# Kernel optimization log

Measured on AMD Instinct MI355X. Metric: run time of the kernel, lower is better.

Reference implementation:

```python
import jax, jax.numpy as jnp
import numpy as np

N_FILTERS = 1024
N_HEADS = 8  # hardcoded h=8 in the original einops.rearrange
LN_EPS = 1e-3  # keras LayerNormalization default epsilon


def setup_inputs() -> dict:
    key = jax.random.key(0)
    k1, k2, k3 = jax.random.split(key, 3)
    B, N, C = 4, 2048, N_FILTERS
    x = jax.random.normal(k1, (B, N, C), dtype=jnp.float32)
    ln_gamma = jnp.ones((C,), dtype=jnp.float32)
    ln_beta = jnp.zeros((C,), dtype=jnp.float32)
    w_qkv = jax.random.normal(k2, (C, 3 * C), dtype=jnp.float32) * 0.02
    w_out = jax.random.normal(k3, (C, C), dtype=jnp.float32) * 0.02
    b_out = jnp.zeros((C,), dtype=jnp.float32)
    return {"x": x, "ln_gamma": ln_gamma, "ln_beta": ln_beta,
            "w_qkv": w_qkv, "w_out": w_out, "b_out": b_out}


def reference(x, ln_gamma, ln_beta, w_qkv, w_out, b_out):
    B, N, C = x.shape
    h = N_HEADS
    hd = C // h
    scale = jnp.asarray(float(C) ** (-0.5), dtype=x.dtype)  # note: full C, as in source

    # LayerNorm over last axis (keras default)
    mu = jnp.mean(x, axis=-1, keepdims=True)
    var = jnp.var(x, axis=-1, keepdims=True)
    xn = (x - mu) / jnp.sqrt(var + LN_EPS) * ln_gamma + ln_beta

    # QKV projection (no bias): [B, N, 3C]
    qkv = jnp.einsum('bnc,cd->bnd', xn, w_qkv)
    # rearrange 'b n (qkv h c) -> qkv b h n c'
    qkv = qkv.reshape(B, N, 3, h, hd).transpose(2, 0, 3, 1, 4)
    q, k, v = qkv[0], qkv[1], qkv[2]

    # attention: [B, h, N, N]
    scores = jnp.einsum('bhnc,bhmc->bhnm', q, k) * scale
    attn = jax.nn.softmax(scores, axis=-1)
    out = jnp.einsum('bhnm,bhmc->bhnc', attn, v)
    # 'b h n c -> b n (h c)'
    out = out.transpose(0, 2, 1, 3).reshape(B, N, C)

    out = jnp.einsum('bnc,cd->bnd', out, w_out) + b_out
    return x + out
```

## Files before the change

kernel.cpp:

```cpp
#include <hip/hip_runtime.h>

typedef _Float16 half8 __attribute__((ext_vector_type(8)));
typedef float floatx4 __attribute__((ext_vector_type(4)));
typedef float floatx16 __attribute__((ext_vector_type(16)));

#define BB 4
#define SEQ 2048
#define CHN 1024
#define NH 8
#define HD 128
#define CQ 3072

__device__ __forceinline__ float bf2f(unsigned short b) {
  unsigned int u = ((unsigned int)b) << 16;
  float f; __builtin_memcpy(&f, &u, 4); return f;
}
__device__ __forceinline__ unsigned short f2bf(float f) {
  unsigned int u; __builtin_memcpy(&u, &f, 4);
  u += 0x7fffu + ((u >> 16) & 1u);
  return (unsigned short)(u >> 16);
}
__device__ __forceinline__ void gl_lds16(const _Float16* g, _Float16* l) {
  __builtin_amdgcn_global_load_lds(
      (const __attribute__((address_space(1))) unsigned int*)(g),
      (__attribute__((address_space(3))) unsigned int*)(l), 16, 0, 0);
}
__device__ __forceinline__ unsigned int pkf16(float a, float b) {
  auto p = __builtin_amdgcn_cvt_pkrtz(a, b);
  unsigned int u; __builtin_memcpy(&u, &p, 4); return u;
}

__global__ __launch_bounds__(256) void detect_k(
    const unsigned int* __restrict__ x, int* __restrict__ flag) {
  __shared__ int bad;
  if (threadIdx.x == 0) bad = 0;
  __syncthreads();
  int b = 0;
#pragma unroll
  for (int i = 0; i < 8; ++i) {
    unsigned int w = x[threadIdx.x * 8 + i];
    float v = bf2f((unsigned short)(w & 0xffffu));
    if (!(fabsf(v) < 1e4f)) b = 1;
  }
  if (b) bad = 1;
  __syncthreads();
  if (threadIdx.x == 0) *flag = bad;
}

__global__ __launch_bounds__(256) void transpose_b2h(
    const void* __restrict__ in, _Float16* __restrict__ out, int R, int C,
    const int* __restrict__ flag) {
  __shared__ _Float16 tile[64][66];
  int isf = *flag;
  int ti = blockIdx.y, tj = blockIdx.x, t = threadIdx.x;
  if (isf) {
    const float* inf = (const float*)in;
#pragma unroll
    for (int i = 0; i < 16; ++i) {
      int lin = i * 256 + t;
      int r = lin >> 6, c = lin & 63;
      tile[r][c] = (_Float16)inf[(size_t)(ti * 64 + r) * C + tj * 64 + c];
    }
  } else {
    const unsigned short* inb = (const unsigned short*)in;
#pragma unroll
    for (int i = 0; i < 16; ++i) {
      int lin = i * 256 + t;
      int r = lin >> 6, c = lin & 63;
      tile[r][c] = (_Float16)bf2f(inb[(size_t)(ti * 64 + r) * C + tj * 64 + c]);
    }
  }
  __syncthreads();
#pragma unroll
  for (int i = 0; i < 16; ++i) {
    int lin = i * 256 + t;
    int c = lin >> 6, r = lin & 63;
    out[(size_t)(tj * 64 + c) * R + ti * 64 + r] = tile[r][c];
  }
}

__global__ __launch_bounds__(256) void ln_k(
    const void* __restrict__ xv, const void* __restrict__ gv,
    const void* __restrict__ bv, _Float16* __restrict__ xn,
    const int* __restrict__ flag) {
  int isf = *flag;
  int row = blockIdx.x, t = threadIdx.x;
  float v0, v1, v2, v3;
  if (isf) {
    const float4 f = *reinterpret_cast<const float4*>((const float*)xv + (size_t)row * CHN + t * 4);
    v0 = f.x; v1 = f.y; v2 = f.z; v3 = f.w;
  } else {
    ushort4 u = *reinterpret_cast<const ushort4*>((const unsigned short*)xv + (size_t)row * CHN + t * 4);
    v0 = bf2f(u.x); v1 = bf2f(u.y); v2 = bf2f(u.z); v3 = bf2f(u.w);
  }
  float s = v0 + v1 + v2 + v3;
  float ss = v0 * v0 + v1 * v1 + v2 * v2 + v3 * v3;
#pragma unroll
  for (int off = 32; off >= 1; off >>= 1) {
    s += __shfl_xor(s, off, 64);
    ss += __shfl_xor(ss, off, 64);
  }
  __shared__ float red[8];
  int wave = t >> 6, lane = t & 63;
  if (lane == 0) { red[wave] = s; red[4 + wave] = ss; }
  __syncthreads();
  s = red[0] + red[1] + red[2] + red[3];
  ss = red[4] + red[5] + red[6] + red[7];
  float mu = s * (1.0f / CHN);
  float var = ss * (1.0f / CHN) - mu * mu;
  float rstd = rsqrtf(var + 1e-3f);
  float g0, g1, g2, g3, b0, b1, b2, b3;
  if (isf) {
    const float4 g = *reinterpret_cast<const float4*>((const float*)gv + t * 4);
    const float4 b = *reinterpret_cast<const float4*>((const float*)bv + t * 4);
    g0 = g.x; g1 = g.y; g2 = g.z; g3 = g.w;
    b0 = b.x; b1 = b.y; b2 = b.z; b3 = b.w;
  } else {
    ushort4 g = *reinterpret_cast<const ushort4*>((const unsigned short*)gv + t * 4);
    ushort4 b = *reinterpret_cast<const ushort4*>((const unsigned short*)bv + t * 4);
    g0 = bf2f(g.x); g1 = bf2f(g.y); g2 = bf2f(g.z); g3 = bf2f(g.w);
    b0 = bf2f(b.x); b1 = bf2f(b.y); b2 = bf2f(b.z); b3 = bf2f(b.w);
  }
  _Float16* o = xn + (size_t)row * CHN + t * 4;
  o[0] = (_Float16)((v0 - mu) * rstd * g0 + b0);
  o[1] = (_Float16)((v1 - mu) * rstd * g1 + b1);
  o[2] = (_Float16)((v2 - mu) * rstd * g2 + b2);
  o[3] = (_Float16)((v3 - mu) * rstd * g3 + b3);
}

template <int EPI>
__global__ __launch_bounds__(256, 3) void gemm_k(
    const _Float16* __restrict__ A, const _Float16* __restrict__ Bt,
    int M, int Nn, int K,
    _Float16* __restrict__ outh, void* __restrict__ outv,
    const void* __restrict__ bias, const void* __restrict__ resid,
    const int* __restrict__ flag) {
  __shared__ _Float16 As[128 * 64];
  __shared__ _Float16 Bs[128 * 64];
  int isf = (EPI == 1) ? *flag : 0;
  int t = threadIdx.x;
  int wave = t >> 6, lane = t & 63, quad = lane >> 4, l15 = lane & 15;
  int wm = wave >> 1, wn = wave & 1;
  size_t arow0 = (size_t)blockIdx.y * 128;
  size_t brow0 = (size_t)blockIdx.x * 128;
  int lr = lane >> 3, lc = lane & 7;
  int gc = lc ^ lr;
  const _Float16* Abase = A + (arow0 + wave * 32 + lr) * (size_t)K + gc * 8;
  const _Float16* Bbase = Bt + (brow0 + wave * 32 + lr) * (size_t)K + gc * 8;
  floatx4 acc[4][4] = {};
  int nkt = K >> 6;
  for (int kt = 0; kt < nkt; ++kt) {
#pragma unroll
    for (int i = 0; i < 4; ++i) {
      gl_lds16(Abase + kt * 64 + (size_t)i * 8 * K, As + (wave * 32 + i * 8) * 64);
      gl_lds16(Bbase + kt * 64 + (size_t)i * 8 * K, Bs + (wave * 32 + i * 8) * 64);
    }
    __syncthreads();
#pragma unroll
    for (int ks = 0; ks < 2; ++ks) {
      half8 af[4], bfr[4];
#pragma unroll
      for (int mt = 0; mt < 4; ++mt) {
        int row = wm * 64 + mt * 16 + l15;
        int slot = (ks * 4 + quad) ^ (l15 & 7);
        af[mt] = *reinterpret_cast<const half8*>(As + row * 64 + slot * 8);
      }
#pragma unroll
      for (int nt = 0; nt < 4; ++nt) {
        int row = wn * 64 + nt * 16 + l15;
        int slot = (ks * 4 + quad) ^ (l15 & 7);
        bfr[nt] = *reinterpret_cast<const half8*>(Bs + row * 64 + slot * 8);
      }
#pragma unroll
      for (int mt = 0; mt < 4; ++mt)
#pragma unroll
        for (int nt = 0; nt < 4; ++nt)
          acc[mt][nt] = __builtin_amdgcn_mfma_f32_16x16x32_f16(af[mt], bfr[nt], acc[mt][nt], 0, 0, 0);
    }
    __syncthreads();
  }
#pragma unroll
  for (int mt = 0; mt < 4; ++mt) {
#pragma unroll
    for (int r = 0; r < 4; ++r) {
      size_t row = arow0 + wm * 64 + mt * 16 + quad * 4 + r;
#pragma unroll
      for (int nt = 0; nt < 4; ++nt) {
        size_t col = brow0 + wn * 64 + nt * 16 + l15;
        float v = acc[mt][nt][r];
        if (EPI == 0) {
          outh[row * Nn + col] = (_Float16)v;
        } else {
          if (isf) {
            v += ((const float*)bias)[col] + ((const float*)resid)[row * Nn + col];
            ((float*)outv)[row * Nn + col] = v;
          } else {
            v += bf2f(((const unsigned short*)bias)[col]) +
                 bf2f(((const unsigned short*)resid)[row * Nn + col]);
            ((unsigned short*)outv)[row * Nn + col] = f2bf(v);
          }
        }
      }
    }
  }
}

__global__ __launch_bounds__(256) void vtrans_k(
    const _Float16* __restrict__ qkv, _Float16* __restrict__ vtr) {
  __shared__ _Float16 tile[64][72];
  int t = threadIdx.x;
  int tok0 = blockIdx.x * 64;
  int hd0 = blockIdx.y * 64;
  int bh = blockIdx.z;
  int b = bh >> 3, h = bh & 7;
  const _Float16* src = qkv + (size_t)b * SEQ * CQ + 2 * CHN + h * HD + hd0;
#pragma unroll
  for (int i = 0; i < 2; ++i) {
    int lin = i * 256 + t;
    int r = lin >> 3, c8 = lin & 7;
    *reinterpret_cast<half8*>(&tile[r][c8 * 8]) =
        *reinterpret_cast<const half8*>(src + (size_t)(tok0 + r) * CQ + c8 * 8);
  }
  __syncthreads();
  _Float16* dst = vtr + ((size_t)bh * HD + hd0) * SEQ + tok0;
#pragma unroll
  for (int i = 0; i < 2; ++i) {
    int lin = i * 256 + t;
    int c = lin >> 3, r8 = lin & 7;
    half8 v;
#pragma unroll
    for (int j = 0; j < 8; ++j) v[j] = tile[r8 * 8 + j][c];
    *reinterpret_cast<half8*>(dst + (size_t)c * SEQ + r8 * 8) = v;
  }
}

__global__ __launch_bounds__(256, 2) void attn_k(
    const _Float16* __restrict__ qkv, const _Float16* __restrict__ vtr,
    _Float16* __restrict__ out) {
  __shared__ _Float16 Ks[2][64 * 128];
  __shared__ _Float16 Vs[2][128 * 64];
  int t = threadIdx.x;
  int wave = t >> 6, lane = t & 63;
  int l31 = lane & 31, hi = lane >> 5;
  int bh = blockIdx.x & 31;
  int qt = blockIdx.x >> 5;
  int b = bh >> 3, h = bh & 7;
  int qbase = qt * 128;
  const _Float16* qp = qkv + (size_t)b * SEQ * CQ + h * HD;
  const _Float16* kp = qp + CHN;
  const _Float16* vtp = vtr + (size_t)bh * HD * SEQ;
  const _Float16 qsc = (_Float16)0.045085299f;
  half8 aq[8];
  {
    const _Float16* qr = qp + (size_t)(qbase + wave * 32 + l31) * CQ + hi * 8;
#pragma unroll
    for (int c = 0; c < 8; ++c) {
      half8 v = *reinterpret_cast<const half8*>(qr + c * 16);
#pragma unroll
      for (int j = 0; j < 8; ++j) v[j] = v[j] * qsc;
      aq[c] = v;
    }
  }
  float l_p = 0.0f;
  floatx16 accO[4] = {};
  int kr = lane >> 4, ks16 = lane & 15;
  int vr = lane >> 3, vs8 = lane & 7;
#pragma unroll
  for (int i = 0; i < 4; ++i) {
    int r = wave * 16 + i * 4 + kr;
    int gcs = ks16 ^ (r & 15);
    gl_lds16(kp + (size_t)r * CQ + gcs * 8, Ks[0] + (wave * 16 + i * 4) * 128);
  }
#pragma unroll
  for (int i = 0; i < 4; ++i) {
    int r = wave * 32 + i * 8 + vr;
    int gcs = vs8 ^ (r & 7);
    gl_lds16(vtp + (size_t)r * SEQ + gcs * 8, Vs[0] + (wave * 32 + i * 8) * 64);
  }
  __syncthreads();
  for (int kt = 0; kt < SEQ / 64; ++kt) {
    if (kt + 1 < SEQ / 64) {
      int kb2 = (kt + 1) * 64;
      _Float16* vdst = Vs[(kt + 1) & 1];
#pragma unroll
      for (int i = 0; i < 4; ++i) {
        int r = wave * 32 + i * 8 + vr;
        int gcs = vs8 ^ (r & 7);
        gl_lds16(vtp + (size_t)r * SEQ + kb2 + gcs * 8, vdst + (wave * 32 + i * 8) * 64);
      }
      const _Float16* kn = kp + (size_t)kb2 * CQ;
      _Float16* kdst = Ks[(kt + 1) & 1];
#pragma unroll
      for (int i = 0; i < 4; ++i) {
        int r = wave * 16 + i * 4 + kr;
        int gcs = ks16 ^ (r & 15);
        gl_lds16(kn + (size_t)r * CQ + gcs * 8, kdst + (wave * 16 + i * 4) * 128);
      }
    }
    const _Float16* kc = Ks[kt & 1];
    floatx16 accST[2] = {};
    __builtin_amdgcn_s_setprio(1);
#pragma unroll
    for (int c = 0; c < 8; ++c) {
#pragma unroll
      for (int sub = 0; sub < 2; ++sub) {
        int row = sub * 32 + l31;
        int chunk = (c * 2 + hi) ^ (row & 15);
        half8 ak = *reinterpret_cast<const half8*>(kc + row * 128 + chunk * 8);
        accST[sub] = __builtin_amdgcn_mfma_f32_32x32x16_f16(ak, aq[c], accST[sub], 0, 0, 0);
      }
    }
    __builtin_amdgcn_s_setprio(0);
    float p0[16], p1[16];
#pragma unroll
    for (int r = 0; r < 16; ++r) p0[r] = __builtin_amdgcn_exp2f(accST[0][r]);
#pragma unroll
    for (int r = 0; r < 16; ++r) p1[r] = __builtin_amdgcn_exp2f(accST[1][r]);
    {
      float s0 = 0, s1 = 0, s2 = 0, s3 = 0;
#pragma unroll
      for (int r = 0; r < 16; r += 4) {
        s0 += p0[r] + p1[r];
        s1 += p0[r + 1] + p1[r + 1];
        s2 += p0[r + 2] + p1[r + 2];
        s3 += p0[r + 3] + p1[r + 3];
      }
      l_p += (s0 + s1) + (s2 + s3);
    }
    const _Float16* vc = Vs[kt & 1];
    __builtin_amdgcn_s_setprio(1);
#pragma unroll
    for (int s = 0; s < 4; ++s) {
      const float* pp = (s & 2) ? p1 : p0;
      int o8 = (s & 1) * 8;
      unsigned int u0 = pkf16(pp[o8 + 0], pp[o8 + 1]);
      unsigned int u1 = pkf16(pp[o8 + 2], pp[o8 + 3]);
      unsigned int w0 = pkf16(pp[o8 + 4], pp[o8 + 5]);
      unsigned int w1 = pkf16(pp[o8 + 6], pp[o8 + 7]);
      asm volatile("v_permlane32_swap_b32 %0, %1" : "+v"(u0), "+v"(w0));
      asm volatile("v_permlane32_swap_b32 %0, %1" : "+v"(u1), "+v"(w1));
      union { unsigned int w[4]; half8 h; } fr;
      fr.w[0] = u0; fr.w[1] = u1; fr.w[2] = w0; fr.w[3] = w1;
#pragma unroll
      for (int dt = 0; dt < 4; ++dt) {
        int row = dt * 32 + l31;
        int chunk = (2 * s + hi) ^ (row & 7);
        half8 bv = *reinterpret_cast<const half8*>(vc + row * 64 + chunk * 8);
        accO[dt] = __builtin_amdgcn_mfma_f32_32x32x16_f16(fr.h, bv, accO[dt], 0, 0, 0);
      }
    }
    __builtin_amdgcn_s_setprio(0);
    __syncthreads();
  }
  l_p += __shfl_xor(l_p, 32, 64);
  float inv[16];
#pragma unroll
  for (int r = 0; r < 16; ++r) {
    int qrow = (r & 3) + 8 * (r >> 2) + 4 * hi;
    inv[r] = 1.0f / __shfl(l_p, qrow, 64);
  }
  _Float16* obase = out + ((size_t)b * SEQ + qbase + wave * 32) * CHN + h * HD;
#pragma unroll
  for (int dt = 0; dt < 4; ++dt)
#pragma unroll
    for (int r = 0; r < 16; ++r) {
      int qrow = (r & 3) + 8 * (r >> 2) + 4 * hi;
      obase[(size_t)qrow * CHN + dt * 32 + l31] = (_Float16)(accO[dt][r] * inv[r]);
    }
}

extern "C" void kernel_launch(void* const* d_in, const int* in_sizes, int n_in,
                              void* d_out, int out_size, void* d_ws, size_t ws_size,
                              hipStream_t stream) {
  (void)in_sizes; (void)n_in; (void)out_size; (void)ws_size;
  const void* x = d_in[0];
  const void* gam = d_in[1];
  const void* bet = d_in[2];
  const void* wqkv = d_in[3];
  const void* wout = d_in[4];
  const void* bout = d_in[5];
  char* ws = (char*)d_ws;
  _Float16* xn    = (_Float16*)(ws);
  _Float16* vtr   = (_Float16*)(ws);
  _Float16* qkv   = (_Float16*)(ws + (size_t)16777216);
  _Float16* aout  = (_Float16*)(ws + (size_t)67108864);
  _Float16* wqkvT = (_Float16*)(ws + (size_t)83886080);
  _Float16* woutT = (_Float16*)(ws + (size_t)90177536);
  int* flag       = (int*)(ws + (size_t)92274688);

  detect_k<<<1, 256, 0, stream>>>((const unsigned int*)x, flag);
  transpose_b2h<<<dim3(CQ / 64, CHN / 64), 256, 0, stream>>>(wqkv, wqkvT, CHN, CQ, flag);
  transpose_b2h<<<dim3(CHN / 64, CHN / 64), 256, 0, stream>>>(wout, woutT, CHN, CHN, flag);
  ln_k<<<dim3(BB * SEQ), 256, 0, stream>>>(x, gam, bet, xn, flag);
  gemm_k<0><<<dim3(CQ / 128, BB * SEQ / 128), 256, 0, stream>>>(
      xn, wqkvT, BB * SEQ, CQ, CHN, qkv, nullptr, nullptr, nullptr, flag);
  vtrans_k<<<dim3(SEQ / 64, HD / 64, BB * NH), 256, 0, stream>>>(qkv, vtr);
  attn_k<<<dim3(BB * NH * (SEQ / 128)), 256, 0, stream>>>(qkv, vtr, aout);
  gemm_k<1><<<dim3(CHN / 128, BB * SEQ / 128), 256, 0, stream>>>(
      aout, woutT, BB * SEQ, CHN, CHN, nullptr, d_out, bout, x, flag);
}
```

Before: 295.0 us.

## Triple-buffer GEMM with 256x128 tiles, 512 threads and swizzled block order

Reworks the projection GEMM into a 256x128 output tile computed by 8 waves, using a K-step of 32. Global-to-LDS loads now go through a three-stage ring buffer whose waits are counted with explicit vmcnt, so loads run two steps ahead of the MFMA work. Blocks are remapped in groups of eight to improve L2 reuse. The attention kernel's LDS index expressions are only rewritten into an equivalent form. The changes add hand-tuned wait counts and larger LDS use, and the swizzle assumes the grid size divides evenly by eight.

```diff
diff --git a/kernel.cpp b/kernel.cpp
--- a/kernel.cpp
+++ b/kernel.cpp
@@ -129,55 +129,77 @@
 }
 
 template <int EPI>
-__global__ __launch_bounds__(256, 3) void gemm_k(
+__global__ __launch_bounds__(512, 2) void gemm_k(
     const _Float16* __restrict__ A, const _Float16* __restrict__ Bt,
     int M, int Nn, int K,
     _Float16* __restrict__ outh, void* __restrict__ outv,
     const void* __restrict__ bias, const void* __restrict__ resid,
     const int* __restrict__ flag) {
-  __shared__ _Float16 As[128 * 64];
-  __shared__ _Float16 Bs[128 * 64];
+  __shared__ _Float16 As[3][256 * 32];
+  __shared__ _Float16 Bs[3][128 * 32];
   int isf = (EPI == 1) ? *flag : 0;
   int t = threadIdx.x;
   int wave = t >> 6, lane = t & 63, quad = lane >> 4, l15 = lane & 15;
   int wm = wave >> 1, wn = wave & 1;
-  size_t arow0 = (size_t)blockIdx.y * 128;
-  size_t brow0 = (size_t)blockIdx.x * 128;
-  int lr = lane >> 3, lc = lane & 7;
-  int gc = lc ^ lr;
-  const _Float16* Abase = A + (arow0 + wave * 32 + lr) * (size_t)K + gc * 8;
-  const _Float16* Bbase = Bt + (brow0 + wave * 32 + lr) * (size_t)K + gc * 8;
+  int nbx = Nn >> 7;
+  int bid = blockIdx.x;
+  int swz = (bid & 7) * ((int)gridDim.x >> 3) + (bid >> 3);
+  int by = swz / nbx;
+  int bx = swz - by * nbx;
+  size_t arow0 = (size_t)by * 256;
+  size_t brow0 = (size_t)bx * 128;
+  int lr = lane >> 2, lc = lane & 3;
+  int gsw = lc ^ ((lr >> 1) & 3);
+  int slotr = quad ^ ((l15 >> 1) & 3);
+
+  auto stage = [&](int kt, int bufi) {
+    int k0 = kt << 5;
+#pragma unroll
+    for (int j = 0; j < 2; ++j) {
+      int r0 = wave * 32 + j * 16;
+      gl_lds16(A + (arow0 + r0 + lr) * (size_t)K + k0 + gsw * 8,
+               &As[bufi][r0 * 32]);
+    }
+    {
+      int r0 = wave * 16;
+      gl_lds16(Bt + (brow0 + r0 + lr) * (size_t)K + k0 + gsw * 8,
+               &Bs[bufi][r0 * 32]);
+    }
+  };
+
   floatx4 acc[4][4] = {};
-  int nkt = K >> 6;
+  int nkt = K >> 5;
+  stage(0, 0);
+  stage(1, 1);
+  stage(2, 2);
+  int bufc = 0;
   for (int kt = 0; kt < nkt; ++kt) {
-#pragma unroll
-    for (int i = 0; i < 4; ++i) {
-      gl_lds16(Abase + kt * 64 + (size_t)i * 8 * K, As + (wave * 32 + i * 8) * 64);
-      gl_lds16(Bbase + kt * 64 + (size_t)i * 8 * K, Bs + (wave * 32 + i * 8) * 64);
-    }
-    __syncthreads();
-#pragma unroll
-    for (int ks = 0; ks < 2; ++ks) {
-      half8 af[4], bfr[4];
-#pragma unroll
-      for (int mt = 0; mt < 4; ++mt) {
-        int row = wm * 64 + mt * 16 + l15;
-        int slot = (ks * 4 + quad) ^ (l15 & 7);
-        af[mt] = *reinterpret_cast<const half8*>(As + row * 64 + slot * 8);
-      }
-#pragma unroll
-      for (int nt = 0; nt < 4; ++nt) {
-        int row = wn * 64 + nt * 16 + l15;
-        int slot = (ks * 4 + quad) ^ (l15 & 7);
-        bfr[nt] = *reinterpret_cast<const half8*>(Bs + row * 64 + slot * 8);
-      }
-#pragma unroll
-      for (int mt = 0; mt < 4; ++mt)
-#pragma unroll
-        for (int nt = 0; nt < 4; ++nt)
-          acc[mt][nt] = __builtin_amdgcn_mfma_f32_16x16x32_f16(af[mt], bfr[nt], acc[mt][nt], 0, 0, 0);
-    }
-    __syncthreads();
+    if (kt < nkt - 2)       asm volatile("s_waitcnt vmcnt(6)" ::: "memory");
+    else if (kt == nkt - 2) asm volatile("s_waitcnt vmcnt(3)" ::: "memory");
+    else                    asm volatile("s_waitcnt vmcnt(0)" ::: "memory");
+    asm volatile("s_waitcnt lgkmcnt(0)" ::: "memory");
+    __builtin_amdgcn_sched_barrier(0);
+    __builtin_amdgcn_s_barrier();
+    __builtin_amdgcn_sched_barrier(0);
+    if (kt + 2 < nkt) {
+      int bn = bufc + 2; if (bn >= 3) bn -= 3;
+      stage(kt + 2, bn);
+    }
+    const _Float16* Ab = As[bufc];
+    const _Float16* Bb = Bs[bufc];
+    half8 af[4], bf[4];
+#pragma unroll
+    for (int mt = 0; mt < 4; ++mt)
+      af[mt] = *reinterpret_cast<const half8*>(Ab + (wm * 64 + mt * 16 + l15) * 32 + slotr * 8);
+#pragma unroll
+    for (int nt = 0; nt < 4; ++nt)
+      bf[nt] = *reinterpret_cast<const half8*>(Bb + (wn * 64 + nt * 16 + l15) * 32 + slotr * 8);
+#pragma unroll
+    for (int mt = 0; mt < 4; ++mt)
+#pragma unroll
+      for (int nt = 0; nt < 4; ++nt)
+        acc[mt][nt] = __builtin_amdgcn_mfma_f32_16x16x32_f16(af[mt], bf[nt], acc[mt][nt], 0, 0, 0);
+    ++bufc; if (bufc == 3) bufc = 0;
   }
 #pragma unroll
   for (int mt = 0; mt < 4; ++mt) {
@@ -306,7 +328,7 @@
       for (int sub = 0; sub < 2; ++sub) {
         int row = sub * 32 + l31;
         int chunk = (c * 2 + hi) ^ (row & 15);
-        half8 ak = *reinterpret_cast<const half8*>(kc + row * 128 + chunk * 8);
+        half8 ak = *reinterpret_cast<const half8*>(kc + (row * 16 + chunk) * 8);
         accST[sub] = __builtin_amdgcn_mfma_f32_32x32x16_f16(ak, aq[c], accST[sub], 0, 0, 0);
       }
     }
@@ -345,7 +367,7 @@
       for (int dt = 0; dt < 4; ++dt) {
         int row = dt * 32 + l31;
         int chunk = (2 * s + hi) ^ (row & 7);
-        half8 bv = *reinterpret_cast<const half8*>(vc + row * 64 + chunk * 8);
+        half8 bv = *reinterpret_cast<const half8*>(vc + (row * 8 + chunk) * 8);
         accO[dt] = __builtin_amdgcn_mfma_f32_32x32x16_f16(fr.h, bv, accO[dt], 0, 0, 0);
       }
     }
@@ -392,10 +414,10 @@
   transpose_b2h<<<dim3(CQ / 64, CHN / 64), 256, 0, stream>>>(wqkv, wqkvT, CHN, CQ, flag);
   transpose_b2h<<<dim3(CHN / 64, CHN / 64), 256, 0, stream>>>(wout, woutT, CHN, CHN, flag);
   ln_k<<<dim3(BB * SEQ), 256, 0, stream>>>(x, gam, bet, xn, flag);
-  gemm_k<0><<<dim3(CQ / 128, BB * SEQ / 128), 256, 0, stream>>>(
+  gemm_k<0><<<dim3((CQ / 128) * (BB * SEQ / 256)), 512, 0, stream>>>(
       xn, wqkvT, BB * SEQ, CQ, CHN, qkv, nullptr, nullptr, nullptr, flag);
   vtrans_k<<<dim3(SEQ / 64, HD / 64, BB * NH), 256, 0, stream>>>(qkv, vtr);
   attn_k<<<dim3(BB * NH * (SEQ / 128)), 256, 0, stream>>>(qkv, vtr, aout);
-  gemm_k<1><<<dim3(CHN / 128, BB * SEQ / 128), 256, 0, stream>>>(
+  gemm_k<1><<<dim3((CHN / 128) * (BB * SEQ / 256)), 512, 0, stream>>>(
       aout, woutT, BB * SEQ, CHN, CHN, nullptr, d_out, bout, x, flag);
 }
```

Measured after the change: 304.2 us. 3.1% more time.

## Restructure GEMM into 128x256 tiles with double-buffered async LDS prefetch

Applied to the files above, without the earlier changes.

Rewrites the shared GEMM kernel to use 512-thread blocks computing 128x256 tiles. It double-buffers the A/B LDS tiles, interleaves global-to-LDS prefetch of the next K slices with MFMA work in four quadrant phases using explicit waitcnt and barriers, and remaps the 1D block index to improve L2 locality. The aim is to hide global load latency and raise data reuse per block. In exchange it doubles LDS use and relies on hand-placed vmcnt counts that must match the number of issued loads. The attention indexing edits are only equivalent arithmetic rewrites.

```diff
diff --git a/kernel.cpp b/kernel.cpp
--- a/kernel.cpp
+++ b/kernel.cpp
@@ -129,80 +129,126 @@
 }
 
 template <int EPI>
-__global__ __launch_bounds__(256, 3) void gemm_k(
+__global__ __launch_bounds__(512, 2) void gemm_k(
     const _Float16* __restrict__ A, const _Float16* __restrict__ Bt,
     int M, int Nn, int K,
     _Float16* __restrict__ outh, void* __restrict__ outv,
     const void* __restrict__ bias, const void* __restrict__ resid,
     const int* __restrict__ flag) {
-  __shared__ _Float16 As[128 * 64];
-  __shared__ _Float16 Bs[128 * 64];
+  __shared__ _Float16 As[2][128 * 64];
+  __shared__ _Float16 Bs[2][256 * 64];
   int isf = (EPI == 1) ? *flag : 0;
   int t = threadIdx.x;
   int wave = t >> 6, lane = t & 63, quad = lane >> 4, l15 = lane & 15;
-  int wm = wave >> 1, wn = wave & 1;
-  size_t arow0 = (size_t)blockIdx.y * 128;
-  size_t brow0 = (size_t)blockIdx.x * 128;
+  int wm = wave >> 2, wn = wave & 3;
+  int nbx = Nn >> 8;
+  int bid = blockIdx.x;
+  int swz = (bid & 7) * ((int)gridDim.x >> 3) + (bid >> 3);
+  int by = swz / nbx, bx = swz - by * nbx;
+  size_t arow0 = (size_t)by * 128;
+  size_t brow0 = (size_t)bx * 256;
   int lr = lane >> 3, lc = lane & 7;
-  int gc = lc ^ lr;
-  const _Float16* Abase = A + (arow0 + wave * 32 + lr) * (size_t)K + gc * 8;
-  const _Float16* Bbase = Bt + (brow0 + wave * 32 + lr) * (size_t)K + gc * 8;
-  floatx4 acc[4][4] = {};
+  int gsw = lc ^ lr;
+
+  auto stageA = [&](int kt, int b, int m2) {
+    int r0 = (wave >> 2) * 64 + m2 * 32 + (wave & 3) * 8;
+    gl_lds16(A + (arow0 + r0 + lr) * (size_t)K + (kt << 6) + gsw * 8,
+             &As[b][r0 * 64]);
+  };
+  auto stageB = [&](int kt, int b, int n2) {
+#pragma unroll
+    for (int j = 0; j < 2; ++j) {
+      int idx = j * 8 + wave;
+      int r0 = (idx >> 2) * 64 + n2 * 32 + (idx & 3) * 8;
+      gl_lds16(Bt + (brow0 + r0 + lr) * (size_t)K + (kt << 6) + gsw * 8,
+               &Bs[b][r0 * 64]);
+    }
+  };
+
+  floatx4 acc[2][2][2][2] = {};
   int nkt = K >> 6;
+  stageA(0, 0, 0); stageA(0, 0, 1); stageB(0, 0, 0); stageB(0, 0, 1);
+  stageA(1, 1, 0); stageB(1, 1, 0);
+  asm volatile("s_waitcnt vmcnt(3)" ::: "memory");
+  asm volatile("s_barrier" ::: "memory");
   for (int kt = 0; kt < nkt; ++kt) {
-#pragma unroll
-    for (int i = 0; i < 4; ++i) {
-      gl_lds16(Abase + kt * 64 + (size_t)i * 8 * K, As + (wave * 32 + i * 8) * 64);
-      gl_lds16(Bbase + kt * 64 + (size_t)i * 8 * K, Bs + (wave * 32 + i * 8) * 64);
-    }
-    __syncthreads();
-#pragma unroll
-    for (int ks = 0; ks < 2; ++ks) {
-      half8 af[4], bfr[4];
-#pragma unroll
-      for (int mt = 0; mt < 4; ++mt) {
-        int row = wm * 64 + mt * 16 + l15;
-        int slot = (ks * 4 + quad) ^ (l15 & 7);
-        af[mt] = *reinterpret_cast<const half8*>(As + row * 64 + slot * 8);
-      }
-#pragma unroll
-      for (int nt = 0; nt < 4; ++nt) {
-        int row = wn * 64 + nt * 16 + l15;
-        int slot = (ks * 4 + quad) ^ (l15 & 7);
-        bfr[nt] = *reinterpret_cast<const half8*>(Bs + row * 64 + slot * 8);
-      }
-#pragma unroll
-      for (int mt = 0; mt < 4; ++mt)
-#pragma unroll
-        for (int nt = 0; nt < 4; ++nt)
-          acc[mt][nt] = __builtin_amdgcn_mfma_f32_16x16x32_f16(af[mt], bfr[nt], acc[mt][nt], 0, 0, 0);
-    }
-    __syncthreads();
-  }
-#pragma unroll
-  for (int mt = 0; mt < 4; ++mt) {
-#pragma unroll
-    for (int r = 0; r < 4; ++r) {
-      size_t row = arow0 + wm * 64 + mt * 16 + quad * 4 + r;
-#pragma unroll
-      for (int nt = 0; nt < 4; ++nt) {
-        size_t col = brow0 + wn * 64 + nt * 16 + l15;
-        float v = acc[mt][nt][r];
-        if (EPI == 0) {
-          outh[row * Nn + col] = (_Float16)v;
-        } else {
-          if (isf) {
-            v += ((const float*)bias)[col] + ((const float*)resid)[row * Nn + col];
-            ((float*)outv)[row * Nn + col] = v;
-          } else {
-            v += bf2f(((const unsigned short*)bias)[col]) +
-                 bf2f(((const unsigned short*)resid)[row * Nn + col]);
-            ((unsigned short*)outv)[row * Nn + col] = f2bf(v);
+    int e = kt & 1;
+    const _Float16* Ab = As[e];
+    const _Float16* Bb = Bs[e];
+#pragma unroll
+    for (int q = 0; q < 4; ++q) {
+      const int m2 = q >> 1, n2 = q & 1;
+      half8 af[2][2], bf[2][2];
+#pragma unroll
+      for (int mt = 0; mt < 2; ++mt) {
+        int R = wm * 64 + m2 * 32 + mt * 16 + l15;
+#pragma unroll
+        for (int ks = 0; ks < 2; ++ks) {
+          int c = ks * 4 + quad;
+          af[mt][ks] = *reinterpret_cast<const half8*>(Ab + R * 64 + ((c ^ (R & 7)) << 3));
+        }
+      }
+#pragma unroll
+      for (int nt = 0; nt < 2; ++nt) {
+        int R = wn * 64 + n2 * 32 + nt * 16 + l15;
+#pragma unroll
+        for (int ks = 0; ks < 2; ++ks) {
+          int c = ks * 4 + quad;
+          bf[nt][ks] = *reinterpret_cast<const half8*>(Bb + R * 64 + ((c ^ (R & 7)) << 3));
+        }
+      }
+      if (q == 0)      { if (kt + 1 < nkt) stageA(kt + 1, e ^ 1, 1); }
+      else if (q == 1) { if (kt + 1 < nkt) stageB(kt + 1, e ^ 1, 1); }
+      else if (q == 2) { if (kt + 2 < nkt) stageA(kt + 2, e, 0); }
+      else             { if (kt + 2 < nkt) stageB(kt + 2, e, 0); }
+      asm volatile("s_barrier" ::: "memory");
+      asm volatile("s_waitcnt lgkmcnt(0)" ::: "memory");
+      __builtin_amdgcn_sched_barrier(0);
+      __builtin_amdgcn_s_setprio(1);
+#pragma unroll
+      for (int mt = 0; mt < 2; ++mt)
+#pragma unroll
+        for (int nt = 0; nt < 2; ++nt)
+#pragma unroll
+          for (int ks = 0; ks < 2; ++ks)
+            acc[m2][n2][mt][nt] = __builtin_amdgcn_mfma_f32_16x16x32_f16(
+                af[mt][ks], bf[nt][ks], acc[m2][n2][mt][nt], 0, 0, 0);
+      __builtin_amdgcn_s_setprio(0);
+      if (q < 3) asm volatile("s_barrier" ::: "memory");
+    }
+    if (kt + 1 < nkt) {
+      if (kt + 2 < nkt) asm volatile("s_waitcnt vmcnt(3)" ::: "memory");
+      else              asm volatile("s_waitcnt vmcnt(0)" ::: "memory");
+      asm volatile("s_barrier" ::: "memory");
+    }
+  }
+#pragma unroll
+  for (int m2 = 0; m2 < 2; ++m2)
+#pragma unroll
+    for (int mt = 0; mt < 2; ++mt)
+#pragma unroll
+      for (int r = 0; r < 4; ++r) {
+        size_t row = arow0 + wm * 64 + m2 * 32 + mt * 16 + quad * 4 + r;
+#pragma unroll
+        for (int n2 = 0; n2 < 2; ++n2)
+#pragma unroll
+          for (int nt = 0; nt < 2; ++nt) {
+            size_t col = brow0 + wn * 64 + n2 * 32 + nt * 16 + l15;
+            float v = acc[m2][n2][mt][nt][r];
+            if (EPI == 0) {
+              outh[row * Nn + col] = (_Float16)v;
+            } else {
+              if (isf) {
+                v += ((const float*)bias)[col] + ((const float*)resid)[row * Nn + col];
+                ((float*)outv)[row * Nn + col] = v;
+              } else {
+                v += bf2f(((const unsigned short*)bias)[col]) +
+                     bf2f(((const unsigned short*)resid)[row * Nn + col]);
+                ((unsigned short*)outv)[row * Nn + col] = f2bf(v);
+              }
+            }
           }
-        }
-      }
-    }
-  }
+      }
 }
 
 __global__ __launch_bounds__(256) void vtrans_k(
@@ -306,7 +352,7 @@
       for (int sub = 0; sub < 2; ++sub) {
         int row = sub * 32 + l31;
         int chunk = (c * 2 + hi) ^ (row & 15);
-        half8 ak = *reinterpret_cast<const half8*>(kc + row * 128 + chunk * 8);
+        half8 ak = *reinterpret_cast<const half8*>(kc + (row * 16 + chunk) * 8);
         accST[sub] = __builtin_amdgcn_mfma_f32_32x32x16_f16(ak, aq[c], accST[sub], 0, 0, 0);
       }
     }
@@ -345,7 +391,7 @@
       for (int dt = 0; dt < 4; ++dt) {
         int row = dt * 32 + l31;
         int chunk = (2 * s + hi) ^ (row & 7);
-        half8 bv = *reinterpret_cast<const half8*>(vc + row * 64 + chunk * 8);
+        half8 bv = *reinterpret_cast<const half8*>(vc + (row * 8 + chunk) * 8);
         accO[dt] = __builtin_amdgcn_mfma_f32_32x32x16_f16(fr.h, bv, accO[dt], 0, 0, 0);
       }
     }
@@ -392,10 +438,10 @@
   transpose_b2h<<<dim3(CQ / 64, CHN / 64), 256, 0, stream>>>(wqkv, wqkvT, CHN, CQ, flag);
   transpose_b2h<<<dim3(CHN / 64, CHN / 64), 256, 0, stream>>>(wout, woutT, CHN, CHN, flag);
   ln_k<<<dim3(BB * SEQ), 256, 0, stream>>>(x, gam, bet, xn, flag);
-  gemm_k<0><<<dim3(CQ / 128, BB * SEQ / 128), 256, 0, stream>>>(
+  gemm_k<0><<<dim3((BB * SEQ / 128) * (CQ / 256)), 512, 0, stream>>>(
       xn, wqkvT, BB * SEQ, CQ, CHN, qkv, nullptr, nullptr, nullptr, flag);
   vtrans_k<<<dim3(SEQ / 64, HD / 64, BB * NH), 256, 0, stream>>>(qkv, vtr);
   attn_k<<<dim3(BB * NH * (SEQ / 128)), 256, 0, stream>>>(qkv, vtr, aout);
-  gemm_k<1><<<dim3(CHN / 128, BB * SEQ / 128), 256, 0, stream>>>(
+  gemm_k<1><<<dim3((BB * SEQ / 128) * (CHN / 256)), 512, 0, stream>>>(
       aout, woutT, BB * SEQ, CHN, CHN, nullptr, d_out, bout, x, flag);
 }
```

Result: slower. 309.5 us (+4.9%).

## Double per-wave query rows in attention to reuse K/V LDS fragments

Applied to the files above, without the earlier changes.

Each wave now processes two 32-row query blocks (256 queries per workgroup) so every K and V fragment read from shared memory feeds two MFMAs. The score, exp and PV loops are restructured per 32-key sub-tile to limit live registers. Grid size halves to 256 workgroups and launch bounds drop to one block per SIMD group. This cuts LDS traffic and K/V global reloads per query, at the cost of higher register pressure, lower occupancy and fewer blocks than compute units for latency hiding.

```diff
diff --git a/kernel.cpp b/kernel.cpp
--- a/kernel.cpp
+++ b/kernel.cpp
@@ -234,7 +234,7 @@
   }
 }
 
-__global__ __launch_bounds__(256, 2) void attn_k(
+__global__ __launch_bounds__(256, 1) void attn_k(
     const _Float16* __restrict__ qkv, const _Float16* __restrict__ vtr,
     _Float16* __restrict__ out) {
   __shared__ _Float16 Ks[2][64 * 128];
@@ -245,24 +245,25 @@
   int bh = blockIdx.x & 31;
   int qt = blockIdx.x >> 5;
   int b = bh >> 3, h = bh & 7;
-  int qbase = qt * 128;
+  int qbase = qt * 256;
   const _Float16* qp = qkv + (size_t)b * SEQ * CQ + h * HD;
   const _Float16* kp = qp + CHN;
   const _Float16* vtp = vtr + (size_t)bh * HD * SEQ;
   const _Float16 qsc = (_Float16)0.045085299f;
-  half8 aq[8];
-  {
-    const _Float16* qr = qp + (size_t)(qbase + wave * 32 + l31) * CQ + hi * 8;
+  half8 aq[2][8];
+#pragma unroll
+  for (int qb = 0; qb < 2; ++qb) {
+    const _Float16* qr = qp + (size_t)(qbase + wave * 64 + qb * 32 + l31) * CQ + hi * 8;
 #pragma unroll
     for (int c = 0; c < 8; ++c) {
       half8 v = *reinterpret_cast<const half8*>(qr + c * 16);
 #pragma unroll
       for (int j = 0; j < 8; ++j) v[j] = v[j] * qsc;
-      aq[c] = v;
-    }
-  }
-  float l_p = 0.0f;
-  floatx16 accO[4] = {};
+      aq[qb][c] = v;
+    }
+  }
+  float l_p0 = 0.0f, l_p1 = 0.0f;
+  floatx16 accO[2][4] = {};
   int kr = lane >> 4, ks16 = lane & 15;
   int vr = lane >> 3, vs8 = lane & 7;
 #pragma unroll
@@ -298,75 +299,94 @@
       }
     }
     const _Float16* kc = Ks[kt & 1];
-    floatx16 accST[2] = {};
-    __builtin_amdgcn_s_setprio(1);
-#pragma unroll
-    for (int c = 0; c < 8; ++c) {
-#pragma unroll
-      for (int sub = 0; sub < 2; ++sub) {
+    const _Float16* vc = Vs[kt & 1];
+#pragma unroll
+    for (int sub = 0; sub < 2; ++sub) {
+      floatx16 a0 = {}, a1 = {};
+      __builtin_amdgcn_s_setprio(1);
+#pragma unroll
+      for (int c = 0; c < 8; ++c) {
         int row = sub * 32 + l31;
         int chunk = (c * 2 + hi) ^ (row & 15);
-        half8 ak = *reinterpret_cast<const half8*>(kc + row * 128 + chunk * 8);
-        accST[sub] = __builtin_amdgcn_mfma_f32_32x32x16_f16(ak, aq[c], accST[sub], 0, 0, 0);
-      }
-    }
-    __builtin_amdgcn_s_setprio(0);
-    float p0[16], p1[16];
-#pragma unroll
-    for (int r = 0; r < 16; ++r) p0[r] = __builtin_amdgcn_exp2f(accST[0][r]);
-#pragma unroll
-    for (int r = 0; r < 16; ++r) p1[r] = __builtin_amdgcn_exp2f(accST[1][r]);
-    {
-      float s0 = 0, s1 = 0, s2 = 0, s3 = 0;
-#pragma unroll
-      for (int r = 0; r < 16; r += 4) {
-        s0 += p0[r] + p1[r];
-        s1 += p0[r + 1] + p1[r + 1];
-        s2 += p0[r + 2] + p1[r + 2];
-        s3 += p0[r + 3] + p1[r + 3];
-      }
-      l_p += (s0 + s1) + (s2 + s3);
-    }
-    const _Float16* vc = Vs[kt & 1];
-    __builtin_amdgcn_s_setprio(1);
-#pragma unroll
-    for (int s = 0; s < 4; ++s) {
-      const float* pp = (s & 2) ? p1 : p0;
-      int o8 = (s & 1) * 8;
-      unsigned int u0 = pkf16(pp[o8 + 0], pp[o8 + 1]);
-      unsigned int u1 = pkf16(pp[o8 + 2], pp[o8 + 3]);
-      unsigned int w0 = pkf16(pp[o8 + 4], pp[o8 + 5]);
-      unsigned int w1 = pkf16(pp[o8 + 6], pp[o8 + 7]);
-      asm volatile("v_permlane32_swap_b32 %0, %1" : "+v"(u0), "+v"(w0));
-      asm volatile("v_permlane32_swap_b32 %0, %1" : "+v"(u1), "+v"(w1));
-      union { unsigned int w[4]; half8 h; } fr;
-      fr.w[0] = u0; fr.w[1] = u1; fr.w[2] = w0; fr.w[3] = w1;
-#pragma unroll
-      for (int dt = 0; dt < 4; ++dt) {
-        int row = dt * 32 + l31;
-        int chunk = (2 * s + hi) ^ (row & 7);
-        half8 bv = *reinterpret_cast<const half8*>(vc + row * 64 + chunk * 8);
-        accO[dt] = __builtin_amdgcn_mfma_f32_32x32x16_f16(fr.h, bv, accO[dt], 0, 0, 0);
-      }
-    }
-    __builtin_amdgcn_s_setprio(0);
+        half8 ak = *reinterpret_cast<const half8*>(kc + (row * 16 + chunk) * 8);
+        a0 = __builtin_amdgcn_mfma_f32_32x32x16_f16(ak, aq[0][c], a0, 0, 0, 0);
+        a1 = __builtin_amdgcn_mfma_f32_32x32x16_f16(ak, aq[1][c], a1, 0, 0, 0);
+      }
+      __builtin_amdgcn_s_setprio(0);
+      float p0[16], p1[16];
+#pragma unroll
+      for (int r = 0; r < 16; ++r) p0[r] = __builtin_amdgcn_exp2f(a0[r]);
+#pragma unroll
+      for (int r = 0; r < 16; ++r) p1[r] = __builtin_amdgcn_exp2f(a1[r]);
+      {
+        float s0 = 0, s1 = 0, s2 = 0, s3 = 0;
+#pragma unroll
+        for (int r = 0; r < 16; r += 4) {
+          s0 += p0[r]; s1 += p0[r + 1]; s2 += p0[r + 2]; s3 += p0[r + 3];
+        }
+        l_p0 += (s0 + s1) + (s2 + s3);
+      }
+      {
+        float s0 = 0, s1 = 0, s2 = 0, s3 = 0;
+#pragma unroll
+        for (int r = 0; r < 16; r += 4) {
+          s0 += p1[r]; s1 += p1[r + 1]; s2 += p1[r + 2]; s3 += p1[r + 3];
+        }
+        l_p1 += (s0 + s1) + (s2 + s3);
+      }
+      __builtin_amdgcn_s_setprio(1);
+#pragma unroll
+      for (int sl = 0; sl < 2; ++sl) {
+        int s = sub * 2 + sl;
+        int o8 = sl * 8;
+        unsigned int u0 = pkf16(p0[o8 + 0], p0[o8 + 1]);
+        unsigned int u1 = pkf16(p0[o8 + 2], p0[o8 + 3]);
+        unsigned int w0 = pkf16(p0[o8 + 4], p0[o8 + 5]);
+        unsigned int w1 = pkf16(p0[o8 + 6], p0[o8 + 7]);
+        asm volatile("v_permlane32_swap_b32 %0, %1" : "+v"(u0), "+v"(w0));
+        asm volatile("v_permlane32_swap_b32 %0, %1" : "+v"(u1), "+v"(w1));
+        union { unsigned int w[4]; half8 h; } fr0;
+        fr0.w[0] = u0; fr0.w[1] = u1; fr0.w[2] = w0; fr0.w[3] = w1;
+        unsigned int x0 = pkf16(p1[o8 + 0], p1[o8 + 1]);
+        unsigned int x1 = pkf16(p1[o8 + 2], p1[o8 + 3]);
+        unsigned int y0 = pkf16(p1[o8 + 4], p1[o8 + 5]);
+        unsigned int y1 = pkf16(p1[o8 + 6], p1[o8 + 7]);
+        asm volatile("v_permlane32_swap_b32 %0, %1" : "+v"(x0), "+v"(y0));
+        asm volatile("v_permlane32_swap_b32 %0, %1" : "+v"(x1), "+v"(y1));
+        union { unsigned int w[4]; half8 h; } fr1;
+        fr1.w[0] = x0; fr1.w[1] = x1; fr1.w[2] = y0; fr1.w[3] = y1;
+#pragma unroll
+        for (int dt = 0; dt < 4; ++dt) {
+          int row = dt * 32 + l31;
+          int chunk = (2 * s + hi) ^ (row & 7);
+          half8 bv = *reinterpret_cast<const half8*>(vc + (row * 8 + chunk) * 8);
+          accO[0][dt] = __builtin_amdgcn_mfma_f32_32x32x16_f16(fr0.h, bv, accO[0][dt], 0, 0, 0);
+          accO[1][dt] = __builtin_amdgcn_mfma_f32_32x32x16_f16(fr1.h, bv, accO[1][dt], 0, 0, 0);
+        }
+      }
+      __builtin_amdgcn_s_setprio(0);
+    }
     __syncthreads();
   }
-  l_p += __shfl_xor(l_p, 32, 64);
-  float inv[16];
-#pragma unroll
-  for (int r = 0; r < 16; ++r) {
-    int qrow = (r & 3) + 8 * (r >> 2) + 4 * hi;
-    inv[r] = 1.0f / __shfl(l_p, qrow, 64);
-  }
-  _Float16* obase = out + ((size_t)b * SEQ + qbase + wave * 32) * CHN + h * HD;
-#pragma unroll
-  for (int dt = 0; dt < 4; ++dt)
+#pragma unroll
+  for (int qb = 0; qb < 2; ++qb) {
+    float l = (qb == 0) ? l_p0 : l_p1;
+    l += __shfl_xor(l, 32, 64);
+    float inv[16];
 #pragma unroll
     for (int r = 0; r < 16; ++r) {
       int qrow = (r & 3) + 8 * (r >> 2) + 4 * hi;
-      obase[(size_t)qrow * CHN + dt * 32 + l31] = (_Float16)(accO[dt][r] * inv[r]);
-    }
+      inv[r] = 1.0f / __shfl(l, qrow, 64);
+    }
+    _Float16* obase = out + ((size_t)b * SEQ + qbase + wave * 64 + qb * 32) * CHN + h * HD;
+#pragma unroll
+    for (int dt = 0; dt < 4; ++dt)
+#pragma unroll
+      for (int r = 0; r < 16; ++r) {
+        int qrow = (r & 3) + 8 * (r >> 2) + 4 * hi;
+        obase[(size_t)qrow * CHN + dt * 32 + l31] = (_Float16)(accO[qb][dt][r] * inv[r]);
+      }
+  }
 }
 
 extern "C" void kernel_launch(void* const* d_in, const int* in_sizes, int n_in,
@@ -395,7 +415,7 @@
   gemm_k<0><<<dim3(CQ / 128, BB * SEQ / 128), 256, 0, stream>>>(
       xn, wqkvT, BB * SEQ, CQ, CHN, qkv, nullptr, nullptr, nullptr, flag);
   vtrans_k<<<dim3(SEQ / 64, HD / 64, BB * NH), 256, 0, stream>>>(qkv, vtr);
-  attn_k<<<dim3(BB * NH * (SEQ / 128)), 256, 0, stream>>>(qkv, vtr, aout);
+  attn_k<<<dim3(BB * NH * (SEQ / 256)), 256, 0, stream>>>(qkv, vtr, aout);
   gemm_k<1><<<dim3(CHN / 128, BB * SEQ / 128), 256, 0, stream>>>(
       aout, woutT, BB * SEQ, CHN, CHN, nullptr, d_out, bout, x, flag);
 }
```

New measurement: 295.8 us. Within noise of the previous version (+0.3%).
